# Optimization experiments

Measured on AMD Instinct MI355X. Metric: run time of the kernel, lower is better.

## Reference

```python
import jax, jax.numpy as jnp
import numpy as np

EMBED_DIM = 768
NUM_HEADS = 12
HEAD_DIM = EMBED_DIM // NUM_HEADS


def setup_inputs() -> dict:
    key = jax.random.key(0)
    ks = jax.random.split(key, 5)
    B, N, D = 8, 1024, EMBED_DIM
    s = 1.0 / np.sqrt(D)
    return {
        "x": jax.random.normal(ks[0], (B, N, D), dtype=jnp.float32),
        "qkv_w": jax.random.uniform(ks[1], (D, 3 * D), jnp.float32, -s, s),  # [in, out]
        "qkv_b": jax.random.uniform(ks[2], (3 * D,), jnp.float32, -s, s),
        "proj_w": jax.random.uniform(ks[3], (D, D), jnp.float32, -s, s),
        "proj_b": jax.random.uniform(ks[4], (D,), jnp.float32, -s, s),
    }


def reference(x, qkv_w, qkv_b, proj_w, proj_b):
    B, N, D = x.shape
    H, Hd = NUM_HEADS, HEAD_DIM
    qkv = x @ qkv_w + qkv_b                          # [B, N, 3D]
    qkv = qkv.reshape(B, N, 3, H, Hd)
    q, k, v = (jnp.moveaxis(qkv, 2, 0)[i].transpose(0, 2, 1, 3) for i in range(3))  # each [B, H, N, Hd]
    scores = jnp.einsum("bhnd,bhmd->bhnm", q, k) / np.sqrt(Hd).astype(x.dtype)
    attn = jax.nn.softmax(scores, axis=-1)           # dropout rate 0.0 -> identity
    out = jnp.einsum("bhnm,bhmd->bhnd", attn, v)     # [B, H, N, Hd]
    out = out.transpose(0, 2, 1, 3).reshape(B, N, D)
    return out @ proj_w + proj_b
```

## Files before the change

### kernel.cpp

```cpp
#include <hip/hip_runtime.h>
#include <hip/hip_bf16.h>

typedef __attribute__((ext_vector_type(8))) short short8;
typedef __attribute__((ext_vector_type(4))) float f32x4;
typedef __attribute__((ext_vector_type(2))) unsigned int uint2v;
typedef unsigned int u32;

#define QSCALE 0.1803368801111204f

__device__ inline ushort f2bf(float f) {
    unsigned int i = __builtin_bit_cast(unsigned int, f);
    unsigned int r = (i + 0x7FFFu + ((i >> 16) & 1u)) >> 16;
    return (ushort)r;
}
__device__ inline u32 pack_bf16(float a, float b) {
    float2 f2; f2.x = a; f2.y = b;
    __hip_bfloat162 h = __float22bfloat162_rn(f2);
    u32 r; __builtin_memcpy(&r, &h, 4);
    return r;
}

__device__ __forceinline__ void gload_lds16(const ushort* g, ushort* l) {
    __builtin_amdgcn_global_load_lds(
        (const __attribute__((address_space(1))) u32*)g,
        (__attribute__((address_space(3))) u32*)l, 16, 0, 0);
}

__global__ __launch_bounds__(256) void convert_f32_bf16(
    const float* __restrict__ in, ushort* __restrict__ outp, int n8)
{
    int idx = blockIdx.x * 256 + threadIdx.x;
    if (idx >= n8) return;
    const float4 u0 = *(const float4*)&in[(size_t)idx * 8];
    const float4 u1 = *(const float4*)&in[(size_t)idx * 8 + 4];
    uint2v a, b;
    a.x = pack_bf16(u0.x, u0.y); a.y = pack_bf16(u0.z, u0.w);
    b.x = pack_bf16(u1.x, u1.y); b.y = pack_bf16(u1.z, u1.w);
    *(uint2v*)&outp[(size_t)idx * 8] = a;
    *(uint2v*)&outp[(size_t)idx * 8 + 4] = b;
}

__global__ __launch_bounds__(256) void transpose_f32_bf16(
    const float* __restrict__ W, ushort* __restrict__ Wt, int K, int N)
{
    __shared__ float tile[32][33];
    const int n0 = blockIdx.x * 32;
    const int k0 = blockIdx.y * 32;
    const int tx = threadIdx.x & 31;
    const int ty = threadIdx.x >> 5;
    for (int i = ty; i < 32; i += 8)
        tile[i][tx] = W[(size_t)(k0 + i) * N + n0 + tx];
    __syncthreads();
    for (int i = ty; i < 32; i += 8)
        Wt[(size_t)(n0 + i) * K + k0 + tx] = f2bf(tile[tx][i]);
}

template <bool OUT_FP32, bool QKV_MODE>
__global__ __launch_bounds__(256) void gemm_bt(
    const ushort* __restrict__ A, const ushort* __restrict__ Bt,
    const float* __restrict__ bias, void* __restrict__ C,
    ushort* __restrict__ Vt, int M, int N, int K, int ldc)
{
    __shared__ __attribute__((aligned(16))) ushort As[128][64];
    __shared__ __attribute__((aligned(16))) ushort Bs[128][64];
    const int tid  = threadIdx.x;
    const int lane = tid & 63;
    const int w    = tid >> 6;
    const int wm   = (w >> 1) * 64;
    const int wn   = (w & 1) * 64;
    const int g    = lane >> 4;
    const int t    = lane & 15;
    const int m0   = blockIdx.y * 128;
    const int n0   = blockIdx.x * 128;

    const int lr = lane >> 3;
    const int pc = lane & 7;

    f32x4 acc[4][4];
#pragma unroll
    for (int i = 0; i < 4; i++)
#pragma unroll
        for (int j = 0; j < 4; j++) acc[i][j] = {0.f, 0.f, 0.f, 0.f};

    const int xorc = t & 7;

    for (int k0 = 0; k0 < K; k0 += 64) {
#pragma unroll
        for (int p = 0; p < 4; p++) {
            const int row = w * 32 + p * 8 + lr;
            const int gc  = pc ^ (row & 7);
            gload_lds16(&A[(size_t)(m0 + row) * K + k0 + gc * 8], &As[w * 32 + p * 8][0]);
            gload_lds16(&Bt[(size_t)(n0 + row) * K + k0 + gc * 8], &Bs[w * 32 + p * 8][0]);
        }
        __syncthreads();
#pragma unroll
        for (int s = 0; s < 2; s++) {
            short8 a[4], b[4];
            const int ca = ((s * 4 + g) ^ xorc) * 8;
#pragma unroll
            for (int i = 0; i < 4; i++)
                a[i] = *(const short8*)&As[wm + i * 16 + t][ca];
#pragma unroll
            for (int j = 0; j < 4; j++)
                b[j] = *(const short8*)&Bs[wn + j * 16 + t][ca];
#pragma unroll
            for (int i = 0; i < 4; i++)
#pragma unroll
                for (int j = 0; j < 4; j++)
                    acc[i][j] = __builtin_amdgcn_mfma_f32_16x16x32_bf16(
                        a[i], b[j], acc[i][j], 0, 0, 0);
        }
        __syncthreads();
    }

#pragma unroll
    for (int j = 0; j < 4; j++) {
        int col = n0 + wn + j * 16 + t;
        float bv = bias[col];
        if (QKV_MODE && col >= 1536) {
            int h = (col - 1536) >> 6, d = col & 63;
#pragma unroll
            for (int i = 0; i < 4; i++) {
                int n = m0 + wm + i * 16 + g * 4;
                int bb = n >> 10, nn = n & 1023;
                uint2v u;
                u.x = pack_bf16(acc[i][j][0] + bv, acc[i][j][1] + bv);
                u.y = pack_bf16(acc[i][j][2] + bv, acc[i][j][3] + bv);
                *(uint2v*)&Vt[(((size_t)bb * 12 + h) * 64 + d) * 1024 + nn] = u;
            }
        } else {
#pragma unroll
            for (int i = 0; i < 4; i++)
#pragma unroll
                for (int r = 0; r < 4; r++) {
                    int row = m0 + wm + i * 16 + g * 4 + r;
                    float val = acc[i][j][r] + bv;
                    if (QKV_MODE && col < 768) val *= QSCALE;
                    if (OUT_FP32) ((float*)C)[(size_t)row * ldc + col] = val;
                    else          ((ushort*)C)[(size_t)row * ldc + col] = f2bf(val);
                }
        }
    }
}

__global__ __launch_bounds__(256) void gemm_bt2(
    const ushort* __restrict__ A, const ushort* __restrict__ Bt,
    const float* __restrict__ bias, float* __restrict__ C,
    int M, int N, int K, int ldc)
{
    __shared__ __attribute__((aligned(16))) ushort As[64][64];
    __shared__ __attribute__((aligned(16))) ushort Bs[128][64];
    const int tid  = threadIdx.x;
    const int lane = tid & 63;
    const int w    = tid >> 6;
    const int g    = lane >> 4;
    const int t    = lane & 15;
    const int m0   = blockIdx.y * 64;
    const int n0   = blockIdx.x * 128;
    const int wn   = w * 32;

    const int lr = lane >> 3;
    const int pc = lane & 7;

    f32x4 acc[4][2];
#pragma unroll
    for (int i = 0; i < 4; i++)
#pragma unroll
        for (int j = 0; j < 2; j++) acc[i][j] = {0.f, 0.f, 0.f, 0.f};

    const int xorc = t & 7;

    for (int k0 = 0; k0 < K; k0 += 64) {
#pragma unroll
        for (int p = 0; p < 2; p++) {
            const int row = w * 16 + p * 8 + lr;
            const int gc  = pc ^ (row & 7);
            gload_lds16(&A[(size_t)(m0 + row) * K + k0 + gc * 8], &As[w * 16 + p * 8][0]);
        }
#pragma unroll
        for (int p = 0; p < 4; p++) {
            const int row = w * 32 + p * 8 + lr;
            const int gc  = pc ^ (row & 7);
            gload_lds16(&Bt[(size_t)(n0 + row) * K + k0 + gc * 8], &Bs[w * 32 + p * 8][0]);
        }
        __syncthreads();
#pragma unroll
        for (int s = 0; s < 2; s++) {
            short8 a[4], b[2];
            const int ca = ((s * 4 + g) ^ xorc) * 8;
#pragma unroll
            for (int i = 0; i < 4; i++)
                a[i] = *(const short8*)&As[i * 16 + t][ca];
#pragma unroll
            for (int j = 0; j < 2; j++)
                b[j] = *(const short8*)&Bs[wn + j * 16 + t][ca];
#pragma unroll
            for (int i = 0; i < 4; i++)
#pragma unroll
                for (int j = 0; j < 2; j++)
                    acc[i][j] = __builtin_amdgcn_mfma_f32_16x16x32_bf16(
                        a[i], b[j], acc[i][j], 0, 0, 0);
        }
        __syncthreads();
    }

#pragma unroll
    for (int j = 0; j < 2; j++) {
        int col = n0 + wn + j * 16 + t;
        float bv = bias[col];
#pragma unroll
        for (int i = 0; i < 4; i++)
#pragma unroll
            for (int r = 0; r < 4; r++) {
                int row = m0 + i * 16 + g * 4 + r;
                C[(size_t)row * ldc + col] = acc[i][j][r] + bv;
            }
    }
}

#define PD 72
__global__ __launch_bounds__(256) void attn_kernel(
    const ushort* __restrict__ qk, const ushort* __restrict__ Vt,
    ushort* __restrict__ out)
{
    __shared__ __attribute__((aligned(16))) ushort Ks[64][64];
    __shared__ __attribute__((aligned(16))) ushort Vs[64][64];
    __shared__ __attribute__((aligned(16))) ushort Ps[4][16][PD];

    const int tid  = threadIdx.x;
    const int lane = tid & 63;
    const int w    = tid >> 6;
    const int g    = lane >> 4;
    const int t    = lane & 15;
    const int q0   = blockIdx.x * 128;
    const int h    = blockIdx.y;
    const int b    = blockIdx.z;

    const int srow = tid >> 3;
    const int pc   = tid & 7;
    const size_t base  = (size_t)b * 1024 * 1536;
    const size_t vbase = ((size_t)b * 12 + h) * 64 * 1024;

    short8 qfrag[2][2];
#pragma unroll
    for (int qf = 0; qf < 2; qf++)
#pragma unroll
        for (int s = 0; s < 2; s++)
            qfrag[qf][s] = *(const short8*)&qk[base +
                (size_t)(q0 + qf * 64 + w * 16 + t) * 1536 + h * 64 + s * 32 + g * 8];

#pragma unroll
    for (int p = 0; p < 2; p++) {
        int r = srow + 32 * p;
        int c = (pc ^ (r & 7)) * 8;
        *(short8*)&Ks[r][c] =
            *(const short8*)&qk[base + (size_t)r * 1536 + 768 + h * 64 + pc * 8];
        *(short8*)&Vs[r][c] =
            *(const short8*)&Vt[vbase + (size_t)r * 1024 + pc * 8];
    }
    short8 kpre[2], vpre[2];
#pragma unroll
    for (int p = 0; p < 2; p++) {
        int r = srow + 32 * p;
        kpre[p] = *(const short8*)&qk[base + (size_t)(64 + r) * 1536 + 768 + h * 64 + pc * 8];
        vpre[p] = *(const short8*)&Vt[vbase + (size_t)r * 1024 + 64 + pc * 8];
    }
    __syncthreads();

    f32x4 o_acc[2][4];
#pragma unroll
    for (int qf = 0; qf < 2; qf++)
#pragma unroll
        for (int j = 0; j < 4; j++) o_acc[qf][j] = {0.f, 0.f, 0.f, 0.f};
    float l_part[2] = {0.f, 0.f};

    for (int kt = 0; kt < 16; kt++) {
        short8 kf[2][4], bv[2][4];
#pragma unroll
        for (int s = 0; s < 2; s++)
#pragma unroll
            for (int j = 0; j < 4; j++) {
                const int row = j * 16 + t;
                const int c = ((s * 4 + g) ^ (t & 7)) * 8;
                kf[s][j] = *(const short8*)&Ks[row][c];
                bv[s][j] = *(const short8*)&Vs[row][c];
            }
        __syncthreads();

        if (kt < 15) {
#pragma unroll
            for (int p = 0; p < 2; p++) {
                int r = srow + 32 * p;
                int c = (pc ^ (r & 7)) * 8;
                *(short8*)&Ks[r][c] = kpre[p];
                *(short8*)&Vs[r][c] = vpre[p];
            }
            if (kt < 14) {
                const int kb = (kt + 2) * 64;
#pragma unroll
                for (int p = 0; p < 2; p++) {
                    int r = srow + 32 * p;
                    kpre[p] = *(const short8*)&qk[base + (size_t)(kb + r) * 1536 + 768 + h * 64 + pc * 8];
                    vpre[p] = *(const short8*)&Vt[vbase + (size_t)r * 1024 + kb + pc * 8];
                }
            }
        }

#pragma unroll
        for (int qf = 0; qf < 2; qf++) {
            f32x4 s_acc[4];
#pragma unroll
            for (int j = 0; j < 4; j++) s_acc[j] = {0.f, 0.f, 0.f, 0.f};
#pragma unroll
            for (int s = 0; s < 2; s++)
#pragma unroll
                for (int j = 0; j < 4; j++)
                    s_acc[j] = __builtin_amdgcn_mfma_f32_16x16x32_bf16(
                        kf[s][j], qfrag[qf][s], s_acc[j], 0, 0, 0);

#pragma unroll
            for (int j = 0; j < 4; j++) {
                float p0 = exp2f(s_acc[j][0]);
                float p1 = exp2f(s_acc[j][1]);
                float p2 = exp2f(s_acc[j][2]);
                float p3 = exp2f(s_acc[j][3]);
                l_part[qf] += (p0 + p1) + (p2 + p3);
                uint2v u;
                u.x = pack_bf16(p0, p1);
                u.y = pack_bf16(p2, p3);
                *(uint2v*)&Ps[w][t][j * 16 + g * 4] = u;
            }

#pragma unroll
            for (int s = 0; s < 2; s++) {
                short8 a = *(const short8*)&Ps[w][t][s * 32 + g * 8];
#pragma unroll
                for (int j = 0; j < 4; j++)
                    o_acc[qf][j] = __builtin_amdgcn_mfma_f32_16x16x32_bf16(
                        a, bv[s][j], o_acc[qf][j], 0, 0, 0);
            }
        }
        __syncthreads();
    }

#pragma unroll
    for (int qf = 0; qf < 2; qf++) {
        float l_tot = l_part[qf];
        l_tot += __shfl_xor(l_tot, 16);
        l_tot += __shfl_xor(l_tot, 32);
        float il[4];
#pragma unroll
        for (int r = 0; r < 4; r++) il[r] = 1.0f / __shfl(l_tot, g * 4 + r);
#pragma unroll
        for (int r = 0; r < 4; r++) {
            int row = q0 + qf * 64 + w * 16 + g * 4 + r;
#pragma unroll
            for (int j = 0; j < 4; j++)
                out[((size_t)(b * 1024 + row)) * 768 + h * 64 + j * 16 + t] =
                    f2bf(o_acc[qf][j][r] * il[r]);
        }
    }
}

extern "C" void kernel_launch(void* const* d_in, const int* in_sizes, int n_in,
                              void* d_out, int out_size, void* d_ws, size_t ws_size,
                              hipStream_t stream)
{
    const float* x      = (const float*)d_in[0];
    const float* qkv_w  = (const float*)d_in[1];
    const float* qkv_b  = (const float*)d_in[2];
    const float* proj_w = (const float*)d_in[3];
    const float* proj_b = (const float*)d_in[4];
    float* out = (float*)d_out;

    char* ws = (char*)d_ws;
    ushort* Wt1 = (ushort*)ws;
    ushort* Wt2 = Wt1 + (size_t)2304 * 768;
    char*   buf = (char*)(Wt2 + (size_t)768 * 768);

    transpose_f32_bf16<<<dim3(72, 24), 256, 0, stream>>>(qkv_w, Wt1, 768, 2304);
    transpose_f32_bf16<<<dim3(24, 24), 256, 0, stream>>>(proj_w, Wt2, 768, 768);

    const size_t wt_bytes   = ((size_t)2304 * 768 + (size_t)768 * 768) * 2;
    const size_t full_bytes = wt_bytes + (size_t)8192 * 768 * 2
                                       + (size_t)8192 * 1536 * 2
                                       + (size_t)8192 * 768 * 2
                                       + (size_t)8192 * 768 * 2;

    if (ws_size >= full_bytes) {
        ushort* xb    = (ushort*)buf;
        ushort* qkO   = xb + (size_t)8192 * 768;
        ushort* VtO   = qkO + (size_t)8192 * 1536;
        ushort* attnO = VtO + (size_t)8192 * 768;
        convert_f32_bf16<<<dim3(3072), 256, 0, stream>>>(x, xb, 786432);
        gemm_bt<false, true><<<dim3(18, 64), 256, 0, stream>>>(
            xb, Wt1, qkv_b, qkO, VtO, 8192, 2304, 768, 1536);
        attn_kernel<<<dim3(8, 12, 8), 256, 0, stream>>>(qkO, VtO, attnO);
        gemm_bt2<<<dim3(6, 128), 256, 0, stream>>>(
            attnO, Wt2, proj_b, out, 8192, 768, 768, 768);
    } else {
        ushort* xbB   = (ushort*)buf;
        ushort* qkB   = xbB + (size_t)1024 * 768;
        ushort* VtB   = qkB + (size_t)1024 * 1536;
        ushort* attnB = VtB + (size_t)1024 * 768;
        for (int b = 0; b < 8; b++) {
            const float* xp = x + (size_t)b * 1024 * 768;
            float* outb = out + (size_t)b * 1024 * 768;
            convert_f32_bf16<<<dim3(384), 256, 0, stream>>>(xp, xbB, 98304);
            gemm_bt<false, true><<<dim3(18, 8), 256, 0, stream>>>(
                xbB, Wt1, qkv_b, qkB, VtB, 1024, 2304, 768, 1536);
            attn_kernel<<<dim3(8, 12, 1), 256, 0, stream>>>(qkB, VtB, attnB);
            gemm_bt2<<<dim3(6, 16), 256, 0, stream>>>(
                attnB, Wt2, proj_b, outb, 1024, 768, 768, 768);
        }
    }
}
```

Measured before the change: 209.1 us.

## Double-buffer K/V tiles in attention and swap grid order for L2 reuse

The attention kernel now keeps two LDS buffers for K and V. It issues the next tile's global loads at the start of each iteration and writes them into the alternate buffer after the compute, which removes one __syncthreads per iteration. All three main kernels also swap their grid axes so that consecutive blocks walk along M, or along (batch, head), which changes the block scheduling order and how operands are shared in L2. The extra LDS doubles K/V shared memory, which may cut occupancy, and the loads now have less time to land before they are consumed.

```diff
diff --git a/kernel.cpp b/kernel.cpp
--- a/kernel.cpp
+++ b/kernel.cpp
@@ -70,8 +70,8 @@
     const int wn   = (w & 1) * 64;
     const int g    = lane >> 4;
     const int t    = lane & 15;
-    const int m0   = blockIdx.y * 128;
-    const int n0   = blockIdx.x * 128;
+    const int m0   = blockIdx.x * 128;
+    const int n0   = blockIdx.y * 128;
 
     const int lr = lane >> 3;
     const int pc = lane & 7;
@@ -155,8 +155,8 @@
     const int w    = tid >> 6;
     const int g    = lane >> 4;
     const int t    = lane & 15;
-    const int m0   = blockIdx.y * 64;
-    const int n0   = blockIdx.x * 128;
+    const int m0   = blockIdx.x * 64;
+    const int n0   = blockIdx.y * 128;
     const int wn   = w * 32;
 
     const int lr = lane >> 3;
@@ -223,8 +223,8 @@
     const ushort* __restrict__ qk, const ushort* __restrict__ Vt,
     ushort* __restrict__ out)
 {
-    __shared__ __attribute__((aligned(16))) ushort Ks[64][64];
-    __shared__ __attribute__((aligned(16))) ushort Vs[64][64];
+    __shared__ __attribute__((aligned(16))) ushort Ks[2][64][64];
+    __shared__ __attribute__((aligned(16))) ushort Vs[2][64][64];
     __shared__ __attribute__((aligned(16))) ushort Ps[4][16][PD];
 
     const int tid  = threadIdx.x;
@@ -232,9 +232,10 @@
     const int w    = tid >> 6;
     const int g    = lane >> 4;
     const int t    = lane & 15;
-    const int q0   = blockIdx.x * 128;
-    const int h    = blockIdx.y;
-    const int b    = blockIdx.z;
+    const int bh   = blockIdx.x;
+    const int b    = bh / 12;
+    const int h    = bh - b * 12;
+    const int q0   = blockIdx.y * 128;
 
     const int srow = tid >> 3;
     const int pc   = tid & 7;
@@ -253,17 +254,10 @@
     for (int p = 0; p < 2; p++) {
         int r = srow + 32 * p;
         int c = (pc ^ (r & 7)) * 8;
-        *(short8*)&Ks[r][c] =
+        *(short8*)&Ks[0][r][c] =
             *(const short8*)&qk[base + (size_t)r * 1536 + 768 + h * 64 + pc * 8];
-        *(short8*)&Vs[r][c] =
+        *(short8*)&Vs[0][r][c] =
             *(const short8*)&Vt[vbase + (size_t)r * 1024 + pc * 8];
-    }
-    short8 kpre[2], vpre[2];
-#pragma unroll
-    for (int p = 0; p < 2; p++) {
-        int r = srow + 32 * p;
-        kpre[p] = *(const short8*)&qk[base + (size_t)(64 + r) * 1536 + 768 + h * 64 + pc * 8];
-        vpre[p] = *(const short8*)&Vt[vbase + (size_t)r * 1024 + 64 + pc * 8];
     }
     __syncthreads();
 
@@ -275,6 +269,19 @@
     float l_part[2] = {0.f, 0.f};
 
     for (int kt = 0; kt < 16; kt++) {
+        const int cur = kt & 1;
+
+        short8 kpre[2], vpre[2];
+        if (kt < 15) {
+            const int kb = (kt + 1) * 64;
+#pragma unroll
+            for (int p = 0; p < 2; p++) {
+                int r = srow + 32 * p;
+                kpre[p] = *(const short8*)&qk[base + (size_t)(kb + r) * 1536 + 768 + h * 64 + pc * 8];
+                vpre[p] = *(const short8*)&Vt[vbase + (size_t)r * 1024 + kb + pc * 8];
+            }
+        }
+
         short8 kf[2][4], bv[2][4];
 #pragma unroll
         for (int s = 0; s < 2; s++)
@@ -282,29 +289,9 @@
             for (int j = 0; j < 4; j++) {
                 const int row = j * 16 + t;
                 const int c = ((s * 4 + g) ^ (t & 7)) * 8;
-                kf[s][j] = *(const short8*)&Ks[row][c];
-                bv[s][j] = *(const short8*)&Vs[row][c];
-            }
-        __syncthreads();
-
-        if (kt < 15) {
-#pragma unroll
-            for (int p = 0; p < 2; p++) {
-                int r = srow + 32 * p;
-                int c = (pc ^ (r & 7)) * 8;
-                *(short8*)&Ks[r][c] = kpre[p];
-                *(short8*)&Vs[r][c] = vpre[p];
-            }
-            if (kt < 14) {
-                const int kb = (kt + 2) * 64;
-#pragma unroll
-                for (int p = 0; p < 2; p++) {
-                    int r = srow + 32 * p;
-                    kpre[p] = *(const short8*)&qk[base + (size_t)(kb + r) * 1536 + 768 + h * 64 + pc * 8];
-                    vpre[p] = *(const short8*)&Vt[vbase + (size_t)r * 1024 + kb + pc * 8];
-                }
-            }
-        }
+                kf[s][j] = *(const short8*)&Ks[cur][row][c];
+                bv[s][j] = *(const short8*)&Vs[cur][row][c];
+            }
 
 #pragma unroll
         for (int qf = 0; qf < 2; qf++) {
@@ -340,6 +327,16 @@
                         a, bv[s][j], o_acc[qf][j], 0, 0, 0);
             }
         }
+
+        if (kt < 15) {
+#pragma unroll
+            for (int p = 0; p < 2; p++) {
+                int r = srow + 32 * p;
+                int c = (pc ^ (r & 7)) * 8;
+                *(short8*)&Ks[cur ^ 1][r][c] = kpre[p];
+                *(short8*)&Vs[cur ^ 1][r][c] = vpre[p];
+            }
+        }
         __syncthreads();
     }
 
@@ -393,10 +390,10 @@
         ushort* VtO   = qkO + (size_t)8192 * 1536;
         ushort* attnO = VtO + (size_t)8192 * 768;
         convert_f32_bf16<<<dim3(3072), 256, 0, stream>>>(x, xb, 786432);
-        gemm_bt<false, true><<<dim3(18, 64), 256, 0, stream>>>(
+        gemm_bt<false, true><<<dim3(64, 18), 256, 0, stream>>>(
             xb, Wt1, qkv_b, qkO, VtO, 8192, 2304, 768, 1536);
-        attn_kernel<<<dim3(8, 12, 8), 256, 0, stream>>>(qkO, VtO, attnO);
-        gemm_bt2<<<dim3(6, 128), 256, 0, stream>>>(
+        attn_kernel<<<dim3(96, 8), 256, 0, stream>>>(qkO, VtO, attnO);
+        gemm_bt2<<<dim3(128, 6), 256, 0, stream>>>(
             attnO, Wt2, proj_b, out, 8192, 768, 768, 768);
     } else {
         ushort* xbB   = (ushort*)buf;
@@ -407,10 +404,10 @@
             const float* xp = x + (size_t)b * 1024 * 768;
             float* outb = out + (size_t)b * 1024 * 768;
             convert_f32_bf16<<<dim3(384), 256, 0, stream>>>(xp, xbB, 98304);
-            gemm_bt<false, true><<<dim3(18, 8), 256, 0, stream>>>(
+            gemm_bt<false, true><<<dim3(8, 18), 256, 0, stream>>>(
                 xbB, Wt1, qkv_b, qkB, VtB, 1024, 2304, 768, 1536);
-            attn_kernel<<<dim3(8, 12, 1), 256, 0, stream>>>(qkB, VtB, attnB);
-            gemm_bt2<<<dim3(6, 16), 256, 0, stream>>>(
+            attn_kernel<<<dim3(12, 8), 256, 0, stream>>>(qkB, VtB, attnB);
+            gemm_bt2<<<dim3(16, 6), 256, 0, stream>>>(
                 attnB, Wt2, proj_b, outb, 1024, 768, 768, 768);
         }
     }
```

Measured after the change: 196.9 us. 1.06x faster.
